# Kernel tuning notes

Measured on AMD Instinct MI355X. Metric: run time of the kernel, lower is better.

## Reference

```python
import jax, jax.numpy as jnp
from jax import lax
import numpy as np


def setup_inputs() -> dict:
    key = jax.random.key(0)
    ks = iter(jax.random.split(key, 48))

    def w(shape):
        fan = shape[0] if len(shape) == 2 else int(np.prod(shape[1:]))
        return jax.random.normal(next(ks), shape, jnp.float32) / np.sqrt(fan)

    def b(n):
        return jax.random.normal(next(ks), (n,), jnp.float32) * 0.01

    T = 16
    return dict(
        search=jax.random.normal(next(ks), (3, 383, 287), jnp.float32),
        exemplars=jax.random.normal(next(ks), (T, 3, 383, 287), jnp.float32),
        # AlexNet features (random-weight stand-in for pretrained)
        aw1=w((64, 3, 11, 11)), ab1=b(64),
        aw2=w((192, 64, 5, 5)), ab2=b(192),
        aw3=w((384, 192, 3, 3)), ab3=b(384),
        aw4=w((256, 384, 3, 3)), ab4=b(256),
        aw5=w((256, 256, 3, 3)), ab5=b(256),
        # conv_deconv: Conv1d(256,256,3,p=1) -> MaxPool1d(88) -> ConvTranspose1d(256,256,88)
        wcd=w((256, 256, 3)), bcd=b(256),
        wt=w((256, 256, 88)), bt=b(256),
        # st_gcn: GCN(256, 512, 256)
        ws1=w((256, 512)), bs1=b(512),
        ws2=w((512, 256)), bs2=b(256),
        # g, h: 1x1 Conv1d(256,256) == linear maps
        wg=w((256, 256)), bg=b(256),
        wh=w((256, 256)), bh=b(256),
        # ct_gcn: GCN(256, 384, 256)
        wc1=w((256, 384)), bc1=b(384),
        wc2=w((384, 256)), bc2=b(256),
    )


def _gct_forward(search, exemplars, aw1, ab1, aw2, ab2, aw3, ab3, aw4, ab4,
                 aw5, ab5, wcd, bcd, wt, bt, ws1, bs1, ws2, bs2,
                 wg, bg, wh, bh, wc1, bc1, wc2, bc2):
    f32 = jnp.float32

    def conv2d(x, w, bias, s, p):
        y = lax.conv_general_dilated(x, w, (s, s), [(p, p), (p, p)],
                                     dimension_numbers=('NCHW', 'OIHW', 'NCHW'))
        return y + bias[None, :, None, None]

    def maxpool(x):  # k=3, s=2, VALID (AlexNet pools)
        return lax.reduce_window(x, -jnp.inf, lax.max, (1, 1, 3, 3), (1, 1, 2, 2), 'VALID')

    def features(x):
        x = maxpool(jax.nn.relu(conv2d(x, aw1, ab1, 4, 2)))
        x = maxpool(jax.nn.relu(conv2d(x, aw2, ab2, 1, 2)))
        x = jax.nn.relu(conv2d(x, aw3, ab3, 1, 1))
        x = jax.nn.relu(conv2d(x, aw4, ab4, 1, 1))
        x = maxpool(jax.nn.relu(conv2d(x, aw5, ab5, 1, 1)))
        return x

    lrelu = lambda v: jax.nn.leaky_relu(v, 0.01)

    X = features(search[None])          # [1,256,11,8]
    Z = features(exemplars)             # [T,256,11,8]
    T = Z.shape[0]
    D = X.shape[1]                      # 256
    M = X.shape[2] * X.shape[3]         # 88
    Xf = X.reshape(D, M)                # [256,88]
    Zf = Z.reshape(T, D, M)             # [T,256,88]

    # conv_deconv branch: conv1d(k=3,p=1) -> global maxpool -> conv_transpose(k=M)
    xc = lax.conv_general_dilated(Xf[None], wcd, (1,), [(1, 1)],
                                  dimension_numbers=('NCH', 'OIH', 'NCH'))[0] + bcd[:, None]
    v = jnp.max(xc, axis=1)                              # [256]
    X_hat = jnp.einsum('i,iok->ok', v, wt) + bt[:, None]  # [256,88]

    # spatiotemporal graph: A[i+T*j, i+T*k]=1 for j!=k; self-loops for t!=0
    TM = T * M
    n = jnp.arange(TM)
    same_t = (n[:, None] % T) == (n[None, :] % T)
    diff_s = (n[:, None] // T) != (n[None, :] // T)
    A1 = (same_t & diff_s).astype(f32) + jnp.diag((n % T != 0).astype(f32))

    # st GCN over TM nodes (node n = t + T*m -> spatial-major flatten)
    nodes = Zf.transpose(2, 0, 1).reshape(TM, D)          # [TM,256]
    h1 = lrelu(A1 @ (nodes @ ws1) + bs1)                  # [TM,512]
    h2 = lrelu(A1 @ (h1 @ ws2) + bs2)                     # [TM,256]
    V1 = jnp.max(h2.reshape(M, T, D), axis=1).T           # temporal max-pool -> [256,88]

    # dynamic cross-track graph: pairwise g/h affinities + row softmax (fused)
    Vx = V1 + X_hat                                       # [256,88]
    G = wg @ Vx + bg[:, None]                             # [256,88]
    Hh = wh @ Vx + bh[:, None]                            # [256,88]
    A2 = jax.nn.softmax(Hh.T @ G, axis=1)                 # [88,88], A2[j,i]=g(i).h(j)

    # ct GCN
    xv = V1.T                                             # [88,256]
    c1 = lrelu(A2 @ (xv @ wc1) + bc1)                     # [88,384]
    V2 = lrelu(A2 @ (c1 @ wc2) + bc2).T                   # [256,88]

    # F.conv2d(X[1,256,11,8], V2[1,256,11,8]) -> full-overlap correlation = scalar
    R = jnp.sum(Xf * V2).reshape(1, 1, 1, 1)
    return R


def reference(search, exemplars, aw1, ab1, aw2, ab2, aw3, ab3, aw4, ab4,
              aw5, ab5, wcd, bcd, wt, bt, ws1, bs1, ws2, bs2,
              wg, bg, wh, bh, wc1, bc1, wc2, bc2):
    return _gct_forward(search, exemplars, aw1, ab1, aw2, ab2, aw3, ab3, aw4, ab4,
                        aw5, ab5, wcd, bcd, wt, bt, ws1, bs1, ws2, bs2,
                        wg, bg, wh, bh, wc1, bc1, wc2, bc2)
```

## Files before the change

### kernel.cpp

```cpp
#include <hip/hip_runtime.h>
#include <hip/hip_bf16.h>
#include <math.h>

#define BATCH 17
#define T_EX 16
#define H0 383
#define W0 287
#define C1 64
#define H1 95
#define W1 71
#define H1P 47
#define W1P 35
#define C2 192
#define H2P 23
#define W2P 17
#define C3 384
#define C45 256
#define H5P 11
#define W5P 8
#define DD 256
#define MM 88
#define TM 1408

#define HP1 389
#define WP1 292

typedef unsigned short ushort_t;
typedef __attribute__((ext_vector_type(8))) short short8;
typedef __attribute__((ext_vector_type(4))) float f32x4;

__device__ __forceinline__ float lrelu(float v) { return v > 0.f ? v : 0.01f * v; }

__device__ __forceinline__ ushort_t f2bf(float f) {
    unsigned int u = __float_as_uint(f);
    unsigned int r = (u + 0x7fffu + ((u >> 16) & 1u)) >> 16;
    return (ushort_t)r;
}
__device__ __forceinline__ float b2f(ushort_t b) {
    return __uint_as_float(((unsigned int)b) << 16);
}
__device__ __forceinline__ short8 ld16(const ushort_t* p) { return *(const short8*)p; }
__device__ __forceinline__ void async_cp16(ushort_t* l, const ushort_t* g) {
    __builtin_amdgcn_global_load_lds(
        (const __attribute__((address_space(1))) void*)g,
        (__attribute__((address_space(3))) void*)l, 16, 0, 0);
}

__global__ void zfill_k(float4* __restrict__ p, int n4) {
    int idx = blockIdx.x * 256 + threadIdx.x;
    if (idx < n4) p[idx] = (float4){0.f, 0.f, 0.f, 0.f};
}

__global__ void prep1_k(const float* __restrict__ search, const float* __restrict__ exemp,
                        ushort_t* __restrict__ out) {
    int idx = blockIdx.x * 256 + threadIdx.x;
    if (idx >= BATCH * H0 * W0) return;
    int ix = idx % W0; int t = idx / W0;
    int iy = t % H0; int b = t / H0;
    const float* src = (b == 0) ? search : exemp + (size_t)(b - 1) * 3 * H0 * W0;
    const int hw = H0 * W0;
    float v0 = src[iy * W0 + ix];
    float v1 = src[hw + iy * W0 + ix];
    float v2 = src[2 * hw + iy * W0 + ix];
    ushort4 o;
    o.x = f2bf(v0); o.y = f2bf(v1); o.z = f2bf(v2); o.w = 0;
    *(ushort4*)&out[(((size_t)b * HP1 + iy + 2) * WP1 + ix + 2) * 4] = o;
}

__global__ void wprep_k(const float* __restrict__ w, ushort_t* __restrict__ out,
                        int KH, int KWl, int KWr, int CINl, int CINr,
                        int NKS, int nch) {
    int idx = blockIdx.x * 256 + threadIdx.x;
    if (idx >= nch) return;
    int c = idx & 255;
    int rest = idx >> 8;
    int ks = rest % NKS;
    int ocb = rest / NKS;
    int k8 = c >> 6, m = c & 63;
    int oc = ocb * 64 + m;
    int KWC = KWl * CINl;
    ushort_t* o = out + (size_t)idx * 8;
#pragma unroll
    for (int j = 0; j < 8; ++j) {
        int kg = ks * 32 + k8 * 8 + j;
        int ky = kg / KWC; int rem = kg - ky * KWC;
        int kx = rem / CINl; int ic = rem - kx * CINl;
        float v = 0.f;
        if (ky < KH && kx < KWr && ic < CINr)
            v = w[(((size_t)oc * CINr + ic) * KH + ky) * KWr + kx];
        o[j] = f2bf(v);
    }
}

__global__ void wprep_gemm_k(const float* __restrict__ ws1, const float* __restrict__ ws2,
                             const float* __restrict__ wcd, ushort_t* __restrict__ WS1T,
                             ushort_t* __restrict__ WS2T, ushort_t* __restrict__ WCDT) {
    int idx = blockIdx.x * 256 + threadIdx.x;
    const float* src; ushort_t* dst; int NKS, mode = 0, sa = 1, sk = 0, base;
    if (idx < 16384)       { src = ws1; dst = WS1T; NKS = 8;  sk = 512; base = idx; }
    else if (idx < 32768)  { src = ws2; dst = WS2T; NKS = 16; sk = 256; base = idx - 16384; }
    else if (idx < 57344)  { src = wcd; dst = WCDT; NKS = 24; mode = 1; base = idx - 32768; }
    else return;
    int c = base & 255;
    int rest = base >> 8;
    int ks = rest % NKS;
    int ocb = rest / NKS;
    int k8 = c >> 6, m = c & 63;
    int oc = ocb * 64 + m;
    ushort_t* o = dst + (size_t)base * 8;
#pragma unroll
    for (int j = 0; j < 8; ++j) {
        int kg = ks * 32 + k8 * 8 + j;
        float v;
        if (mode == 0) v = src[(size_t)oc * sa + (size_t)kg * sk];
        else           v = src[(size_t)oc * 768 + (kg & 255) * 3 + (kg >> 8)];
        o[j] = f2bf(v);
    }
}

template <int STRIDE>
__global__ __launch_bounds__(256) void conv_mfma7(
    const ushort_t* __restrict__ inp, const ushort_t* __restrict__ wt,
    const float* __restrict__ bias, ushort_t* __restrict__ out,
    int Hp, int Wp, int C, int Wout, int HW, int Ntot, int NKS2, int KWl,
    int OHp, int OWp, int OPAD, int COUT) {
    const int tid = threadIdx.x;
    const int wv = tid >> 6, lane = tid & 63;
    const int quad = lane >> 4, l16 = lane & 15;
    const int n_blk = blockIdx.x * 64;
    const int ocb = blockIdx.y;

    __shared__ ushort_t Bs[2][4096];
    __shared__ int offs[432];

    const int KWC = KWl * C;
    for (int g = tid; g < NKS2 * 8; g += 256) {
        int kg = g * 8;
        int ky = kg / KWC; int rem = kg - ky * KWC;
        int kx = rem / C; int c8 = rem - kx * C;
        offs[g] = (ky * Wp + kx) * C + c8;
    }

    int n0 = n_blk + lane; if (n0 >= Ntot) n0 = Ntot - 1;
    const int b0 = n0 / HW, p0 = n0 - b0 * HW;
    const int oy0 = p0 / Wout, ox0 = p0 - oy0 * Wout;
    const ushort_t* src0 = inp + (size_t)b0 * Hp * Wp * C +
                           (size_t)(oy0 * STRIDE * Wp + ox0 * STRIDE) * C;

    f32x4 acc[4];
#pragma unroll
    for (int cn = 0; cn < 4; ++cn) acc[cn] = (f32x4){0.f, 0.f, 0.f, 0.f};

    const ushort_t* wblk = wt + (size_t)ocb * (size_t)NKS2 * 4096;
    const ushort_t* wp = wblk + (size_t)(quad * 64 + wv * 16 + l16) * 8;

    __syncthreads();

    {
        const int o0 = offs[wv], o1 = offs[4 + wv];
        async_cp16(&Bs[0][tid * 8], src0 + o0);
        async_cp16(&Bs[0][2048 + tid * 8], src0 + o1);
    }
    short8 ac0 = ld16(wp);
    short8 ac1 = ld16(wp + 2048);

    for (int ks2 = 0; ks2 < NKS2; ++ks2) {
        const int cur = ks2 & 1;
        if (ks2 + 1 < NKS2) {
            const int o0 = offs[(ks2 + 1) * 8 + wv], o1 = offs[(ks2 + 1) * 8 + 4 + wv];
            ushort_t* bb = &Bs[cur ^ 1][0];
            async_cp16(bb + tid * 8, src0 + o0);
            async_cp16(bb + 2048 + tid * 8, src0 + o1);
            asm volatile("s_waitcnt vmcnt(2)");
        } else {
            asm volatile("s_waitcnt vmcnt(0)");
        }
        __builtin_amdgcn_s_barrier();
        __builtin_amdgcn_sched_barrier(0);
#pragma unroll
        for (int h = 0; h < 2; ++h) {
            const short8 af = h ? ac1 : ac0;
#pragma unroll
            for (int cn = 0; cn < 4; ++cn) {
                const short8 bfr = *(const short8*)&Bs[cur][h * 2048 + (quad * 64 + cn * 16 + l16) * 8];
                acc[cn] = __builtin_amdgcn_mfma_f32_16x16x32_bf16(af, bfr, acc[cn], 0, 0, 0);
            }
        }
        __builtin_amdgcn_sched_barrier(0);
        __builtin_amdgcn_s_barrier();
        if (ks2 + 1 < NKS2) {
            const ushort_t* wp2 = wp + (size_t)(ks2 + 1) * 4096;
            ac0 = ld16(wp2);
            ac1 = ld16(wp2 + 2048);
        }
    }

    const int oc0 = ocb * 64 + wv * 16 + quad * 4;
    const float bi0 = bias[oc0], bi1 = bias[oc0 + 1], bi2 = bias[oc0 + 2], bi3 = bias[oc0 + 3];
#pragma unroll
    for (int cn = 0; cn < 4; ++cn) {
        int n = n_blk + cn * 16 + l16;
        if (n < Ntot) {
            int bb = n / HW; int pix = n - bb * HW;
            int y = pix / Wout, x = pix - y * Wout;
            size_t base = (((size_t)bb * OHp + y + OPAD) * OWp + x + OPAD) * COUT + oc0;
            ushort4 o;
            o.x = f2bf(fmaxf(acc[cn][0] + bi0, 0.f));
            o.y = f2bf(fmaxf(acc[cn][1] + bi1, 0.f));
            o.z = f2bf(fmaxf(acc[cn][2] + bi2, 0.f));
            o.w = f2bf(fmaxf(acc[cn][3] + bi3, 0.f));
            *(ushort4*)&out[base] = o;
        }
    }
}

template <int MODE, bool HASBIAS, bool SC1>
__global__ __launch_bounds__(256) void gemm_mfma3(
    const ushort_t* __restrict__ Bsrc, const ushort_t* __restrict__ wt,
    const float* __restrict__ bias, float* __restrict__ out,
    int RS, int N, int NKS, int sn, int sc) {
    const int tid = threadIdx.x;
    const int wv = tid >> 6, lane = tid & 63;
    const int quad = lane >> 4, l16 = lane & 15;
    const int n_blk = blockIdx.x * 64;
    const int ocb = blockIdx.y;

    __shared__ ushort_t Bs[2][2048];

    int n_g = n_blk + lane;
    int n_gc = n_g < N ? n_g : N - 1;
    int row = (MODE == 1) ? (1 + (n_gc & 15)) * MM + (n_gc >> 4) : n_gc;
    const size_t base0 = (size_t)row * RS;

    f32x4 acc[4];
#pragma unroll
    for (int cn = 0; cn < 4; ++cn) acc[cn] = (f32x4){0.f, 0.f, 0.f, 0.f};

    const ushort_t* wblk = wt + (size_t)ocb * NKS * 2048;
    const int afrag = (quad * 64 + wv * 16 + l16) * 8;

    short8 a0 = ld16(wblk + afrag);
    *(short8*)&Bs[0][tid * 8] = ld16(Bsrc + base0 + wv * 8);
    __syncthreads();

    for (int ks = 0; ks < NKS; ++ks) {
        const int cur = ks & 1, nxt = cur ^ 1;
        short8 a1, bn;
        const bool more = (ks + 1 < NKS);
        if (more) {
            a1 = ld16(wblk + (ks + 1) * 2048 + afrag);
            bn = ld16(Bsrc + base0 + (ks + 1) * 32 + wv * 8);
        }
#pragma unroll
        for (int cn = 0; cn < 4; ++cn) {
            const short8 bfr = *(const short8*)&Bs[cur][(quad * 64 + cn * 16 + l16) * 8];
            acc[cn] = __builtin_amdgcn_mfma_f32_16x16x32_bf16(a0, bfr, acc[cn], 0, 0, 0);
        }
        if (more) *(short8*)&Bs[nxt][tid * 8] = bn;
        a0 = a1;
        __syncthreads();
    }

    const int oc0 = ocb * 64 + wv * 16 + quad * 4;
    float bb[4] = {0.f, 0.f, 0.f, 0.f};
    if (HASBIAS) { bb[0] = bias[oc0]; bb[1] = bias[oc0+1]; bb[2] = bias[oc0+2]; bb[3] = bias[oc0+3]; }
#pragma unroll
    for (int cn = 0; cn < 4; ++cn) {
        int n = n_blk + cn * 16 + l16;
        if (n < N) {
            if (SC1) {
                float4 o;
                o.x = acc[cn][0] + bb[0]; o.y = acc[cn][1] + bb[1];
                o.z = acc[cn][2] + bb[2]; o.w = acc[cn][3] + bb[3];
                *(float4*)&out[(size_t)n * sn + oc0] = o;
            } else {
#pragma unroll
                for (int reg = 0; reg < 4; ++reg)
                    out[(size_t)n * sn + (size_t)(oc0 + reg) * sc] = acc[cn][reg] + bb[reg];
            }
        }
    }
}

__global__ void pool_nhwc(const ushort_t* __restrict__ in, ushort_t* __restrict__ out,
                          int C, int Hin, int Win, int Hout, int Wout,
                          int OHp, int OWp, int OPAD) {
    int total = BATCH * C * Hout * Wout;
    int idx = blockIdx.x * 256 + threadIdx.x;
    if (idx >= total) return;
    int c = idx % C; int r = idx / C;
    int x = r % Wout; r /= Wout;
    int y = r % Hout; int b = r / Hout;
    const int rs = Win * C;
    const ushort_t* p = in + (((size_t)b * Hin + 2 * y) * Win + 2 * x) * C + c;
    float m = b2f(p[0]);
    m = fmaxf(m, b2f(p[C])); m = fmaxf(m, b2f(p[2 * C]));
    m = fmaxf(m, b2f(p[rs])); m = fmaxf(m, b2f(p[rs + C])); m = fmaxf(m, b2f(p[rs + 2 * C]));
    m = fmaxf(m, b2f(p[2 * rs])); m = fmaxf(m, b2f(p[2 * rs + C])); m = fmaxf(m, b2f(p[2 * rs + 2 * C]));
    out[(((size_t)b * OHp + y + OPAD) * OWp + x + OPAD) * C + c] = f2bf(m);
}

__global__ void pool5_k(const ushort_t* __restrict__ in, float* __restrict__ P,
                        ushort_t* __restrict__ PB, ushort_t* __restrict__ XfPad) {
    int total = BATCH * 256 * MM;
    int idx = blockIdx.x * 256 + threadIdx.x;
    if (idx >= total) return;
    int c = idx % 256; int r = idx / 256;
    int x = r % W5P; r /= W5P;
    int y = r % H5P; int b = r / H5P;
    const int rs = W2P * 256;
    const ushort_t* p = in + (((size_t)b * H2P + 2 * y) * W2P + 2 * x) * 256 + c;
    float m = b2f(p[0]);
    m = fmaxf(m, b2f(p[256])); m = fmaxf(m, b2f(p[512]));
    m = fmaxf(m, b2f(p[rs])); m = fmaxf(m, b2f(p[rs + 256])); m = fmaxf(m, b2f(p[rs + 512]));
    m = fmaxf(m, b2f(p[2 * rs])); m = fmaxf(m, b2f(p[2 * rs + 256])); m = fmaxf(m, b2f(p[2 * rs + 512]));
    int mm = y * W5P + x;
    size_t o = ((size_t)b * MM + mm) * 256 + c;
    P[o] = m;
    ushort_t mb = f2bf(m);
    PB[o] = mb;
    if (b == 0) XfPad[(size_t)(mm + 1) * 256 + c] = mb;
}

__global__ void vmax_k(const float* __restrict__ xc, float* __restrict__ v) {
    int c = blockIdx.x * 64 + threadIdx.x;
    float m = -INFINITY;
    for (int j = 0; j < MM; ++j) m = fmaxf(m, xc[(size_t)c * MM + j]);
    v[c] = m;
}

__global__ void xhat_k(const float* __restrict__ v, const float* __restrict__ wt,
                       const float* __restrict__ bt, float* __restrict__ xhat) {
    __shared__ float lv[256];
    for (int j = threadIdx.x; j < 256; j += 256) lv[j] = v[j];
    __syncthreads();
    int idx = blockIdx.x * 256 + threadIdx.x;
    if (idx >= DD * MM) return;
    int k = idx % MM, o = idx / MM;
    float acc = bt[o];
    for (int i = 0; i < 256; ++i) acc = fmaf(lv[i], wt[(i * 256 + o) * MM + k], acc);
    xhat[idx] = acc;
}

__global__ void s1_k(const float* __restrict__ Y1, float* __restrict__ S1) {
    int idx = blockIdx.x * 256 + threadIdx.x;
    if (idx >= T_EX * 512) return;
    int c = idx % 512, t = idx / 512;
    float acc = 0.f;
    for (int m = 0; m < MM; ++m) acc += Y1[(m * T_EX + t) * 512 + c];
    S1[idx] = acc;
}

__global__ void h1_k(const float* __restrict__ Y1, const float* __restrict__ S1,
                     const float* __restrict__ bs1, ushort_t* __restrict__ h1b) {
    int idx = blockIdx.x * 256 + threadIdx.x;
    if (idx >= TM * 512) return;
    int c = idx % 512; int n = idx / 512;
    int t = n % T_EX;
    float val = S1[t * 512 + c] + bs1[c];
    if (t == 0) val -= Y1[idx];
    h1b[idx] = f2bf(lrelu(val));
}

__global__ void s2_k(const float* __restrict__ Y2, float* __restrict__ S2) {
    int idx = blockIdx.x * 256 + threadIdx.x;
    if (idx >= T_EX * 256) return;
    int c = idx % 256, t = idx / 256;
    float acc = 0.f;
    for (int m = 0; m < MM; ++m) acc += Y2[(m * T_EX + t) * 256 + c];
    S2[idx] = acc;
}

__global__ void h2_k(const float* __restrict__ Y2, const float* __restrict__ S2,
                     const float* __restrict__ bs2, float* __restrict__ h2) {
    int idx = blockIdx.x * 256 + threadIdx.x;
    if (idx >= TM * 256) return;
    int c = idx % 256; int n = idx / 256;
    int t = n % T_EX;
    float val = S2[t * 256 + c] + bs2[c];
    if (t == 0) val -= Y2[idx];
    h2[idx] = lrelu(val);
}

__global__ void v1vx_k(const float* __restrict__ h2, const float* __restrict__ xhat,
                       float* __restrict__ V1, float* __restrict__ Vx) {
    int idx = blockIdx.x * 256 + threadIdx.x;
    if (idx >= DD * MM) return;
    int m = idx % MM, d = idx / MM;
    float mx = -INFINITY;
    for (int t = 0; t < T_EX; ++t) mx = fmaxf(mx, h2[(m * T_EX + t) * 256 + d]);
    V1[idx] = mx;
    Vx[idx] = mx + xhat[idx];
}

__global__ void lin88_k(const float* __restrict__ Wg, const float* __restrict__ bg,
                        const float* __restrict__ Wh, const float* __restrict__ bh,
                        const float* __restrict__ Vin, float* __restrict__ Gout,
                        float* __restrict__ Hout) {
    int idx = blockIdx.x * 256 + threadIdx.x;
    if (idx >= DD * MM) return;
    const float* W = blockIdx.y ? Wh : Wg;
    const float* bias = blockIdx.y ? bh : bg;
    float* out = blockIdx.y ? Hout : Gout;
    int m = idx % MM, o = idx / MM;
    const float* wr = W + o * 256;
    float acc = bias[o];
    for (int i = 0; i < 256; ++i) acc = fmaf(wr[i], Vin[i * MM + m], acc);
    out[idx] = acc;
}

__global__ void smsm_k(const float* __restrict__ Hh, const float* __restrict__ G,
                       float* __restrict__ A2) {
    int j = blockIdx.x;
    int tid = threadIdx.x;
    __shared__ float row[96];
    __shared__ float red[128];
    for (int i = tid; i < MM; i += 128) {
        float acc = 0.f;
        for (int c = 0; c < 256; ++c) acc = fmaf(Hh[c * MM + j], G[c * MM + i], acc);
        row[i] = acc;
    }
    __syncthreads();
    float val = (tid < MM) ? row[tid] : -INFINITY;
    red[tid] = val; __syncthreads();
    for (int s = 64; s > 0; s >>= 1) {
        if (tid < s) red[tid] = fmaxf(red[tid], red[tid + s]);
        __syncthreads();
    }
    float mx = red[0]; __syncthreads();
    float e = (tid < MM) ? expf(val - mx) : 0.f;
    red[tid] = e; __syncthreads();
    for (int s = 64; s > 0; s >>= 1) {
        if (tid < s) red[tid] += red[tid + s];
        __syncthreads();
    }
    float inv = 1.f / red[0];
    if (tid < MM) A2[j * MM + tid] = e * inv;
}

__global__ void t1_k(const float* __restrict__ V1, const float* __restrict__ wc1,
                     float* __restrict__ t1) {
    int idx = blockIdx.x * 256 + threadIdx.x;
    if (idx >= MM * 384) return;
    int c = idx % 384, m = idx / 384;
    float acc = 0.f;
    for (int d = 0; d < 256; ++d) acc = fmaf(V1[d * MM + m], wc1[d * 384 + c], acc);
    t1[idx] = acc;
}

__global__ void c1_k(const float* __restrict__ A2, const float* __restrict__ t1,
                     const float* __restrict__ bc1, float* __restrict__ c1) {
    int idx = blockIdx.x * 256 + threadIdx.x;
    if (idx >= MM * 384) return;
    int c = idx % 384, j = idx / 384;
    float acc = bc1[c];
    for (int i = 0; i < MM; ++i) acc = fmaf(A2[j * MM + i], t1[i * 384 + c], acc);
    c1[idx] = lrelu(acc);
}

__global__ void t2_k(const float* __restrict__ c1, const float* __restrict__ wc2,
                     float* __restrict__ t2) {
    int idx = blockIdx.x * 256 + threadIdx.x;
    if (idx >= MM * 256) return;
    int c = idx % 256, m = idx / 256;
    const float* cr = c1 + m * 384;
    float acc = 0.f;
    for (int d = 0; d < 384; ++d) acc = fmaf(cr[d], wc2[d * 256 + c], acc);
    t2[idx] = acc;
}

__global__ void v2_k(const float* __restrict__ A2, const float* __restrict__ t2,
                     const float* __restrict__ bc2, float* __restrict__ V2m) {
    int idx = blockIdx.x * 256 + threadIdx.x;
    if (idx >= MM * 256) return;
    int c = idx % 256, j = idx / 256;
    float acc = bc2[c];
    for (int i = 0; i < MM; ++i) acc = fmaf(A2[j * MM + i], t2[i * 256 + c], acc);
    V2m[idx] = lrelu(acc);
}

__global__ void final_k(const float* __restrict__ Xf2, const float* __restrict__ V2m,
                        float* __restrict__ out) {
    __shared__ float red[256];
    float acc = 0.f;
    for (int idx = threadIdx.x; idx < DD * MM; idx += 256)
        acc = fmaf(Xf2[idx], V2m[idx], acc);
    red[threadIdx.x] = acc; __syncthreads();
    for (int s = 128; s > 0; s >>= 1) {
        if (threadIdx.x < s) red[threadIdx.x] += red[threadIdx.x + s];
        __syncthreads();
    }
    if (threadIdx.x == 0) out[0] = red[0];
}

extern "C" void kernel_launch(void* const* d_in, const int* in_sizes, int n_in,
                              void* d_out, int out_size, void* d_ws, size_t ws_size,
                              hipStream_t stream) {
    const float* search = (const float*)d_in[0];
    const float* exemp  = (const float*)d_in[1];
    const float* aw1 = (const float*)d_in[2];  const float* ab1 = (const float*)d_in[3];
    const float* aw2 = (const float*)d_in[4];  const float* ab2 = (const float*)d_in[5];
    const float* aw3 = (const float*)d_in[6];  const float* ab3 = (const float*)d_in[7];
    const float* aw4 = (const float*)d_in[8];  const float* ab4 = (const float*)d_in[9];
    const float* aw5 = (const float*)d_in[10]; const float* ab5 = (const float*)d_in[11];
    const float* wcd = (const float*)d_in[12]; const float* bcd = (const float*)d_in[13];
    const float* wt  = (const float*)d_in[14]; const float* bt  = (const float*)d_in[15];
    const float* ws1 = (const float*)d_in[16]; const float* bs1 = (const float*)d_in[17];
    const float* ws2 = (const float*)d_in[18]; const float* bs2 = (const float*)d_in[19];
    const float* wg  = (const float*)d_in[20]; const float* bg  = (const float*)d_in[21];
    const float* wh  = (const float*)d_in[22]; const float* bh  = (const float*)d_in[23];
    const float* wc1 = (const float*)d_in[24]; const float* bc1 = (const float*)d_in[25];
    const float* wc2 = (const float*)d_in[26]; const float* bc2 = (const float*)d_in[27];

    float* ws = (float*)d_ws;
    float* R1 = ws;
    float* R2 = ws + 3870720;
    float* R3 = ws + 7544832;
    float* Wg = ws + 8628864;

    ushort_t* in1p  = (ushort_t*)R1;
    ushort_t* c1out = (ushort_t*)R2;
    ushort_t* p1out = (ushort_t*)R3;
    ushort_t* c2out = (ushort_t*)R1;
    ushort_t* p2out = (ushort_t*)R2;
    ushort_t* c3out = (ushort_t*)(R2 + 775200);
    ushort_t* c4out = (ushort_t*)R1;
    ushort_t* c5out = (ushort_t*)R3;
    ushort_t* WT    = (ushort_t*)Wg;

    zfill_k<<<(965500 + 255) / 256, 256, 0, stream>>>((float4*)R1, 965500);
    prep1_k<<<(BATCH * H0 * W0 + 255) / 256, 256, 0, stream>>>(search, exemp, in1p);
    wprep_k<<<(4608 + 255) / 256, 256, 0, stream>>>(aw1, WT, 11, 12, 11, 4, 3, 18, 4608);
    conv_mfma7<4><<<dim3(1792, 1), 256, 0, stream>>>(
        in1p, WT, ab1, c1out, HP1, WP1, 4, W1, H1 * W1, BATCH * H1 * W1, 9, 12, H1, W1, 0, 64);
    zfill_k<<<(270504 + 255) / 256, 256, 0, stream>>>((float4*)R3, 270504);
    pool_nhwc<<<(BATCH * 64 * H1P * W1P + 255) / 256, 256, 0, stream>>>(
        c1out, p1out, 64, H1, W1, H1P, W1P, 51, 39, 2);
    wprep_k<<<(38400 + 255) / 256, 256, 0, stream>>>(aw2, WT, 5, 5, 5, 64, 64, 50, 38400);
    conv_mfma7<1><<<dim3(437, 3), 256, 0, stream>>>(
        p1out, WT, ab2, c2out, 51, 39, 64, W1P, H1P * W1P, BATCH * H1P * W1P, 25, 5, H1P, W1P, 0, 192);
    zfill_k<<<(581400 + 255) / 256, 256, 0, stream>>>((float4*)R2, 581400);
    pool_nhwc<<<(BATCH * 192 * H2P * W2P + 255) / 256, 256, 0, stream>>>(
        c2out, p2out, 192, H1P, W1P, H2P, W2P, 25, 19, 1);
    wprep_k<<<(82944 + 255) / 256, 256, 0, stream>>>(aw3, WT, 3, 3, 3, 192, 192, 54, 82944);
    conv_mfma7<1><<<dim3(104, 6), 256, 0, stream>>>(
        p2out, WT, ab3, c3out, 25, 19, 192, W2P, H2P * W2P, BATCH * H2P * W2P, 27, 3, 25, 19, 1, 384);
    zfill_k<<<(258400 + 255) / 256, 256, 0, stream>>>((float4*)R1, 258400);
    wprep_k<<<(110592 + 255) / 256, 256, 0, stream>>>(aw4, WT, 3, 3, 3, 384, 384, 108, 110592);
    conv_mfma7<1><<<dim3(104, 4), 256, 0, stream>>>(
        c3out, WT, ab4, c4out, 25, 19, 384, W2P, H2P * W2P, BATCH * H2P * W2P, 54, 3, 25, 19, 1, 256);
    wprep_k<<<(73728 + 255) / 256, 256, 0, stream>>>(aw5, WT, 3, 3, 3, 256, 256, 72, 73728);
    conv_mfma7<1><<<dim3(104, 4), 256, 0, stream>>>(
        c4out, WT, ab5, c5out, 25, 19, 256, W2P, H2P * W2P, BATCH * H2P * W2P, 36, 3, H2P, W2P, 0, 256);

    float*    P      = R1 + 2417664;
    ushort_t* PB     = (ushort_t*)(R1 + 2800640);
    ushort_t* XfPad  = (ushort_t*)(R1 + 2992128);
    float*    xc     = R1 + 3003648;

    ushort_t* WS1T = (ushort_t*)Wg;
    ushort_t* WS2T = (ushort_t*)(Wg + 65536);
    ushort_t* WCDT = (ushort_t*)(Wg + 131072);
    wprep_gemm_k<<<(57344 + 255) / 256, 256, 0, stream>>>(ws1, ws2, wcd, WS1T, WS2T, WCDT);

    pool5_k<<<(BATCH * 256 * MM + 255) / 256, 256, 0, stream>>>(c5out, P, PB, XfPad);
    float* Xf2 = P;

    float* v_   = R1 + 0;
    float* xhat = R1 + 1024;
    float* Y1   = R1 + 23552;
    float* S1   = R1 + 744448;
    ushort_t* h1b = (ushort_t*)(R1 + 752640);
    float* Y2   = R1 + 1473536;
    float* S2   = R1 + 1833984;
    float* h2   = R1 + 1838080;
    float* V1   = R1 + 2198528;
    float* Vx   = R1 + 2221056;
    float* G    = R1 + 2243584;
    float* Hh   = R1 + 2266112;
    float* A2   = R1 + 2296832;
    float* t1   = R1 + 2305024;
    float* c1   = R1 + 2338816;
    float* t2   = R1 + 2372608;
    float* V2m  = R1 + 2395136;

    gemm_mfma3<0, true, false><<<dim3(2, 4), 256, 0, stream>>>(
        XfPad, WCDT, bcd, xc, 256, MM, 24, 1, MM);
    vmax_k<<<4, 64, 0, stream>>>(xc, v_);
    xhat_k<<<(DD * MM + 255) / 256, 256, 0, stream>>>(v_, wt, bt, xhat);

    gemm_mfma3<1, false, true><<<dim3(22, 8), 256, 0, stream>>>(
        PB, WS1T, nullptr, Y1, 256, TM, 8, 512, 1);
    s1_k<<<(T_EX * 512 + 255) / 256, 256, 0, stream>>>(Y1, S1);
    h1_k<<<(TM * 512 + 255) / 256, 256, 0, stream>>>(Y1, S1, bs1, h1b);
    gemm_mfma3<0, false, true><<<dim3(22, 4), 256, 0, stream>>>(
        h1b, WS2T, nullptr, Y2, 512, TM, 16, 256, 1);
    s2_k<<<(T_EX * 256 + 255) / 256, 256, 0, stream>>>(Y2, S2);
    h2_k<<<(TM * 256 + 255) / 256, 256, 0, stream>>>(Y2, S2, bs2, h2);
    v1vx_k<<<(DD * MM + 255) / 256, 256, 0, stream>>>(h2, xhat, V1, Vx);

    lin88_k<<<dim3((DD * MM + 255) / 256, 2), 256, 0, stream>>>(wg, bg, wh, bh, Vx, G, Hh);
    smsm_k<<<MM, 128, 0, stream>>>(Hh, G, A2);

    t1_k<<<(MM * 384 + 255) / 256, 256, 0, stream>>>(V1, wc1, t1);
    c1_k<<<(MM * 384 + 255) / 256, 256, 0, stream>>>(A2, t1, bc1, c1);
    t2_k<<<(MM * 256 + 255) / 256, 256, 0, stream>>>(c1, wc2, t2);
    v2_k<<<(MM * 256 + 255) / 256, 256, 0, stream>>>(A2, t2, bc2, V2m);

    final_k<<<1, 256, 0, stream>>>(Xf2, V2m, (float*)d_out);
}
```

Measured before the change: 555.6 us.

## Retile conv kernels to 64x128 register-direct MFMA with software prefetch

```diff
diff --git a/kernel.cpp b/kernel.cpp
--- a/kernel.cpp
+++ b/kernel.cpp
@@ -40,11 +40,6 @@
     return __uint_as_float(((unsigned int)b) << 16);
 }
 __device__ __forceinline__ short8 ld16(const ushort_t* p) { return *(const short8*)p; }
-__device__ __forceinline__ void async_cp16(ushort_t* l, const ushort_t* g) {
-    __builtin_amdgcn_global_load_lds(
-        (const __attribute__((address_space(1))) void*)g,
-        (__attribute__((address_space(3))) void*)l, 16, 0, 0);
-}
 
 __global__ void zfill_k(float4* __restrict__ p, int n4) {
     int idx = blockIdx.x * 256 + threadIdx.x;
@@ -118,8 +113,37 @@
     }
 }
 
-template <int STRIDE>
-__global__ __launch_bounds__(256) void conv_mfma7(
+__device__ __forceinline__ void conv_ld(short8 (&A)[2][2], short8 (&B)[2][4],
+                                        const ushort_t* wblk,
+                                        const ushort_t* const (&bp)[4],
+                                        const int* offs, int ks, int quad) {
+    const ushort_t* wk = wblk + (size_t)ks * 4096;
+    A[0][0] = ld16(wk);
+    A[0][1] = ld16(wk + 128);
+    A[1][0] = ld16(wk + 2048);
+    A[1][1] = ld16(wk + 2176);
+    const int g = ks * 8 + quad;
+    const int o0 = offs[g], o1 = offs[g + 4];
+#pragma unroll
+    for (int cn = 0; cn < 4; ++cn) {
+        B[0][cn] = ld16(bp[cn] + o0);
+        B[1][cn] = ld16(bp[cn] + o1);
+    }
+}
+
+__device__ __forceinline__ void conv_mm(f32x4 (&acc)[2][4], const short8 (&A)[2][2],
+                                        const short8 (&B)[2][4]) {
+#pragma unroll
+    for (int h = 0; h < 2; ++h)
+#pragma unroll
+        for (int cn = 0; cn < 4; ++cn) {
+            acc[0][cn] = __builtin_amdgcn_mfma_f32_16x16x32_bf16(A[h][0], B[h][cn], acc[0][cn], 0, 0, 0);
+            acc[1][cn] = __builtin_amdgcn_mfma_f32_16x16x32_bf16(A[h][1], B[h][cn], acc[1][cn], 0, 0, 0);
+        }
+}
+
+template <int STRIDE, bool PREFB, int MINW>
+__global__ __launch_bounds__(256, MINW) void conv_mfma8(
     const ushort_t* __restrict__ inp, const ushort_t* __restrict__ wt,
     const float* __restrict__ bias, ushort_t* __restrict__ out,
     int Hp, int Wp, int C, int Wout, int HW, int Ntot, int NKS2, int KWl,
@@ -127,12 +151,11 @@
     const int tid = threadIdx.x;
     const int wv = tid >> 6, lane = tid & 63;
     const int quad = lane >> 4, l16 = lane & 15;
-    const int n_blk = blockIdx.x * 64;
+    const int wr = wv >> 1, wc = wv & 1;
+    const int n_blk = blockIdx.x * 128;
     const int ocb = blockIdx.y;
 
-    __shared__ ushort_t Bs[2][4096];
     __shared__ int offs[432];
-
     const int KWC = KWl * C;
     for (int g = tid; g < NKS2 * 8; g += 256) {
         int kg = g * 8;
@@ -140,76 +163,65 @@
         int kx = rem / C; int c8 = rem - kx * C;
         offs[g] = (ky * Wp + kx) * C + c8;
     }
-
-    int n0 = n_blk + lane; if (n0 >= Ntot) n0 = Ntot - 1;
-    const int b0 = n0 / HW, p0 = n0 - b0 * HW;
-    const int oy0 = p0 / Wout, ox0 = p0 - oy0 * Wout;
-    const ushort_t* src0 = inp + (size_t)b0 * Hp * Wp * C +
-                           (size_t)(oy0 * STRIDE * Wp + ox0 * STRIDE) * C;
-
-    f32x4 acc[4];
-#pragma unroll
-    for (int cn = 0; cn < 4; ++cn) acc[cn] = (f32x4){0.f, 0.f, 0.f, 0.f};
-
-    const ushort_t* wblk = wt + (size_t)ocb * (size_t)NKS2 * 4096;
-    const ushort_t* wp = wblk + (size_t)(quad * 64 + wv * 16 + l16) * 8;
-
     __syncthreads();
 
-    {
-        const int o0 = offs[wv], o1 = offs[4 + wv];
-        async_cp16(&Bs[0][tid * 8], src0 + o0);
-        async_cp16(&Bs[0][2048 + tid * 8], src0 + o1);
-    }
-    short8 ac0 = ld16(wp);
-    short8 ac1 = ld16(wp + 2048);
-
-    for (int ks2 = 0; ks2 < NKS2; ++ks2) {
-        const int cur = ks2 & 1;
-        if (ks2 + 1 < NKS2) {
-            const int o0 = offs[(ks2 + 1) * 8 + wv], o1 = offs[(ks2 + 1) * 8 + 4 + wv];
-            ushort_t* bb = &Bs[cur ^ 1][0];
-            async_cp16(bb + tid * 8, src0 + o0);
-            async_cp16(bb + 2048 + tid * 8, src0 + o1);
-            asm volatile("s_waitcnt vmcnt(2)");
-        } else {
-            asm volatile("s_waitcnt vmcnt(0)");
+    const ushort_t* bp[4];
+#pragma unroll
+    for (int cn = 0; cn < 4; ++cn) {
+        int n = n_blk + wc * 64 + cn * 16 + l16;
+        if (n >= Ntot) n = Ntot - 1;
+        int b = n / HW, p = n - b * HW;
+        int oy = p / Wout, ox = p - oy * Wout;
+        bp[cn] = inp + (size_t)b * Hp * Wp * C +
+                 (size_t)(oy * STRIDE * Wp + ox * STRIDE) * C;
+    }
+
+    f32x4 acc[2][4];
+#pragma unroll
+    for (int m = 0; m < 2; ++m)
+#pragma unroll
+        for (int cn = 0; cn < 4; ++cn) acc[m][cn] = (f32x4){0.f, 0.f, 0.f, 0.f};
+
+    const ushort_t* wblk = wt + (size_t)ocb * (size_t)NKS2 * 4096 +
+                           (size_t)(quad * 64 + wr * 32 + l16) * 8;
+
+    if constexpr (!PREFB) {
+        for (int ks = 0; ks < NKS2; ++ks) {
+            short8 A[2][2], B[2][4];
+            conv_ld(A, B, wblk, bp, offs, ks, quad);
+            conv_mm(acc, A, B);
         }
-        __builtin_amdgcn_s_barrier();
-        __builtin_amdgcn_sched_barrier(0);
-#pragma unroll
-        for (int h = 0; h < 2; ++h) {
-            const short8 af = h ? ac1 : ac0;
-#pragma unroll
-            for (int cn = 0; cn < 4; ++cn) {
-                const short8 bfr = *(const short8*)&Bs[cur][h * 2048 + (quad * 64 + cn * 16 + l16) * 8];
-                acc[cn] = __builtin_amdgcn_mfma_f32_16x16x32_bf16(af, bfr, acc[cn], 0, 0, 0);
-            }
+    } else {
+        short8 aA[2][2], bA[2][4], aB[2][2], bB[2][4];
+        conv_ld(aA, bA, wblk, bp, offs, 0, quad);
+        int ks = 0;
+        for (; ks + 2 <= NKS2; ks += 2) {
+            if (ks + 1 < NKS2) conv_ld(aB, bB, wblk, bp, offs, ks + 1, quad);
+            conv_mm(acc, aA, bA);
+            if (ks + 2 < NKS2) conv_ld(aA, bA, wblk, bp, offs, ks + 2, quad);
+            conv_mm(acc, aB, bB);
         }
-        __builtin_amdgcn_sched_barrier(0);
-        __builtin_amdgcn_s_barrier();
-        if (ks2 + 1 < NKS2) {
-            const ushort_t* wp2 = wp + (size_t)(ks2 + 1) * 4096;
-            ac0 = ld16(wp2);
-            ac1 = ld16(wp2 + 2048);
-        }
-    }
-
-    const int oc0 = ocb * 64 + wv * 16 + quad * 4;
-    const float bi0 = bias[oc0], bi1 = bias[oc0 + 1], bi2 = bias[oc0 + 2], bi3 = bias[oc0 + 3];
+        if (ks < NKS2) conv_mm(acc, aA, bA);
+    }
+
+    const int oc0 = ocb * 64 + wr * 32 + quad * 4;
 #pragma unroll
     for (int cn = 0; cn < 4; ++cn) {
-        int n = n_blk + cn * 16 + l16;
+        int n = n_blk + wc * 64 + cn * 16 + l16;
         if (n < Ntot) {
             int bb = n / HW; int pix = n - bb * HW;
             int y = pix / Wout, x = pix - y * Wout;
-            size_t base = (((size_t)bb * OHp + y + OPAD) * OWp + x + OPAD) * COUT + oc0;
-            ushort4 o;
-            o.x = f2bf(fmaxf(acc[cn][0] + bi0, 0.f));
-            o.y = f2bf(fmaxf(acc[cn][1] + bi1, 0.f));
-            o.z = f2bf(fmaxf(acc[cn][2] + bi2, 0.f));
-            o.w = f2bf(fmaxf(acc[cn][3] + bi3, 0.f));
-            *(ushort4*)&out[base] = o;
+            size_t base = (((size_t)bb * OHp + y + OPAD) * OWp + x + OPAD) * COUT;
+#pragma unroll
+            for (int am = 0; am < 2; ++am) {
+                const int oc = oc0 + am * 16;
+                ushort4 o;
+                o.x = f2bf(fmaxf(acc[am][cn][0] + bias[oc], 0.f));
+                o.y = f2bf(fmaxf(acc[am][cn][1] + bias[oc + 1], 0.f));
+                o.z = f2bf(fmaxf(acc[am][cn][2] + bias[oc + 2], 0.f));
+                o.w = f2bf(fmaxf(acc[am][cn][3] + bias[oc + 3], 0.f));
+                *(ushort4*)&out[base + oc] = o;
+            }
         }
     }
 }
@@ -531,26 +543,26 @@
     zfill_k<<<(965500 + 255) / 256, 256, 0, stream>>>((float4*)R1, 965500);
     prep1_k<<<(BATCH * H0 * W0 + 255) / 256, 256, 0, stream>>>(search, exemp, in1p);
     wprep_k<<<(4608 + 255) / 256, 256, 0, stream>>>(aw1, WT, 11, 12, 11, 4, 3, 18, 4608);
-    conv_mfma7<4><<<dim3(1792, 1), 256, 0, stream>>>(
+    conv_mfma8<4, false, 4><<<dim3(896, 1), 256, 0, stream>>>(
         in1p, WT, ab1, c1out, HP1, WP1, 4, W1, H1 * W1, BATCH * H1 * W1, 9, 12, H1, W1, 0, 64);
     zfill_k<<<(270504 + 255) / 256, 256, 0, stream>>>((float4*)R3, 270504);
     pool_nhwc<<<(BATCH * 64 * H1P * W1P + 255) / 256, 256, 0, stream>>>(
         c1out, p1out, 64, H1, W1, H1P, W1P, 51, 39, 2);
     wprep_k<<<(38400 + 255) / 256, 256, 0, stream>>>(aw2, WT, 5, 5, 5, 64, 64, 50, 38400);
-    conv_mfma7<1><<<dim3(437, 3), 256, 0, stream>>>(
+    conv_mfma8<1, false, 4><<<dim3(219, 3), 256, 0, stream>>>(
         p1out, WT, ab2, c2out, 51, 39, 64, W1P, H1P * W1P, BATCH * H1P * W1P, 25, 5, H1P, W1P, 0, 192);
     zfill_k<<<(581400 + 255) / 256, 256, 0, stream>>>((float4*)R2, 581400);
     pool_nhwc<<<(BATCH * 192 * H2P * W2P + 255) / 256, 256, 0, stream>>>(
         c2out, p2out, 192, H1P, W1P, H2P, W2P, 25, 19, 1);
     wprep_k<<<(82944 + 255) / 256, 256, 0, stream>>>(aw3, WT, 3, 3, 3, 192, 192, 54, 82944);
-    conv_mfma7<1><<<dim3(104, 6), 256, 0, stream>>>(
+    conv_mfma8<1, true, 2><<<dim3(52, 6), 256, 0, stream>>>(
         p2out, WT, ab3, c3out, 25, 19, 192, W2P, H2P * W2P, BATCH * H2P * W2P, 27, 3, 25, 19, 1, 384);
     zfill_k<<<(258400 + 255) / 256, 256, 0, stream>>>((float4*)R1, 258400);
     wprep_k<<<(110592 + 255) / 256, 256, 0, stream>>>(aw4, WT, 3, 3, 3, 384, 384, 108, 110592);
-    conv_mfma7<1><<<dim3(104, 4), 256, 0, stream>>>(
+    conv_mfma8<1, true, 2><<<dim3(52, 4), 256, 0, stream>>>(
         c3out, WT, ab4, c4out, 25, 19, 384, W2P, H2P * W2P, BATCH * H2P * W2P, 54, 3, 25, 19, 1, 256);
     wprep_k<<<(73728 + 255) / 256, 256, 0, stream>>>(aw5, WT, 3, 3, 3, 256, 256, 72, 73728);
-    conv_mfma7<1><<<dim3(104, 4), 256, 0, stream>>>(
+    conv_mfma8<1, true, 2><<<dim3(52, 4), 256, 0, stream>>>(
         c4out, WT, ab5, c5out, 25, 19, 256, W2P, H2P * W2P, BATCH * H2P * W2P, 36, 3, H2P, W2P, 0, 256);
 
     float*    P      = R1 + 2417664;
```

After: 651.5 us. 17.2% more time.
